# Kernel tuning notes

Measured on AMD Instinct MI355X. Metric: run time of the kernel, lower is better.

Reference implementation:

```python
import jax, jax.numpy as jnp
import numpy as np

B, S, D, H = 2, 2048, 1024, 16
HD = D // H
SCALE = HD ** -0.5


def setup_inputs() -> dict:
    key = jax.random.key(0)
    k1, k2, k3 = jax.random.split(key, 3)
    x = jax.random.normal(k1, (B, S, D), dtype=jnp.float32)
    # causal mask: True = masked (as used by masked_fill)
    mask = jnp.triu(jnp.ones((S, S), dtype=bool), k=1)
    w_qkv = jax.random.normal(k2, (D, 3 * D), dtype=jnp.float32) * (D ** -0.5)
    b_qkv = jnp.zeros((3 * D,), dtype=jnp.float32)
    w_out = jax.random.normal(k3, (D, D), dtype=jnp.float32) * (D ** -0.5)
    b_out = jnp.zeros((D,), dtype=jnp.float32)
    return {"x": x, "mask": mask, "w_qkv": w_qkv, "b_qkv": b_qkv,
            "w_out": w_out, "b_out": b_out}


def reference(x, mask, w_qkv, b_qkv, w_out, b_out):
    # qkv projection and split
    qkv = x @ w_qkv + b_qkv                     # [b, s, 3D]
    q, k, v = jnp.split(qkv, 3, axis=-1)
    # b s (h d) -> b h s d
    def to_heads(t):
        return t.reshape(B, S, H, HD).transpose(0, 2, 1, 3)
    q, k, v = to_heads(q), to_heads(k), to_heads(v)
    # attention scores [b, h, s, s]
    scores = jnp.einsum('bhqd,bhkd->bhqk', q, k) * SCALE
    scores = jnp.where(mask, -jnp.inf, scores)
    attn = jax.nn.softmax(scores, axis=-1)      # dropout is identity (eval)
    out = jnp.einsum('bhqk,bhkd->bhqd', attn, v)
    out = out.transpose(0, 2, 1, 3).reshape(B, S, D)  # b h s d -> b s (h d)
    out = out @ w_out + b_out                   # out dropout identity (eval)
    return (out, k, v)
```

## Files before the change

### kernel.cpp

```cpp
#include <hip/hip_runtime.h>
#include <hip/hip_bf16.h>

typedef short bf16x8 __attribute__((ext_vector_type(8)));
typedef short u16x4v __attribute__((ext_vector_type(4)));
typedef float f32x4  __attribute__((ext_vector_type(4)));
typedef unsigned short u16;
typedef unsigned int   u32;

#define NB   2
#define NS   2048
#define ND   1024
#define NH   16
#define NHD  64
#define N3   3072
#define NM   4096

__device__ __forceinline__ u16 f2bf(float f) {
    u32 u;
    __builtin_memcpy(&u, &f, 4);
    u += 0x7fffu + ((u >> 16) & 1u);
    return (u16)(u >> 16);
}
__device__ __forceinline__ bf16x8 load8f(const float* f) {
    float4 a = *(const float4*)f;
    float4 b = *(const float4*)(f + 4);
    bf16x8 r;
    r[0] = (short)f2bf(a.x); r[1] = (short)f2bf(a.y);
    r[2] = (short)f2bf(a.z); r[3] = (short)f2bf(a.w);
    r[4] = (short)f2bf(b.x); r[5] = (short)f2bf(b.y);
    r[6] = (short)f2bf(b.z); r[7] = (short)f2bf(b.w);
    return r;
}
__device__ __forceinline__ void gload_lds16(const void* g, void* l) {
    __builtin_amdgcn_global_load_lds(
        (const __attribute__((address_space(1))) u32*)g,
        (__attribute__((address_space(3))) u32*)l, 16, 0, 0);
}

__global__ __launch_bounds__(256) void prep_cvt(
    const float* __restrict__ X, u16* __restrict__ Xb,
    const float* __restrict__ Wqkv, u16* __restrict__ WqkvT,
    const float* __restrict__ Wout, u16* __restrict__ WoutT)
{
    __shared__ float t[32][33];
    const int b = blockIdx.x;
    if (b < 2048) {
        const int i = (b * 256 + threadIdx.x) * 8;
        *(bf16x8*)(Xb + i) = load8f(X + i);
        return;
    }
    const float* in; u16* outp; int R, C, tIdx;
    if (b < 5120) { in = Wqkv; outp = WqkvT; R = ND; C = N3; tIdx = b - 2048; }
    else          { in = Wout; outp = WoutT; R = ND; C = ND; tIdx = b - 5120; }
    const int nbc = C >> 5;
    const int r0 = (tIdx / nbc) << 5;
    const int c0 = (tIdx % nbc) << 5;
    const int tr = threadIdx.x >> 3, tc = (threadIdx.x & 7) << 2;
    const float4 v = *(const float4*)(in + (size_t)(r0 + tr) * C + c0 + tc);
    t[tr][tc] = v.x; t[tr][tc + 1] = v.y; t[tr][tc + 2] = v.z; t[tr][tc + 3] = v.w;
    __syncthreads();
    u16x4v ov;
    ov[0] = (short)f2bf(t[tc + 0][tr]); ov[1] = (short)f2bf(t[tc + 1][tr]);
    ov[2] = (short)f2bf(t[tc + 2][tr]); ov[3] = (short)f2bf(t[tc + 3][tr]);
    *(u16x4v*)(outp + (size_t)(c0 + tr) * R + r0 + tc) = ov;
}

template<bool BF>
__global__ __launch_bounds__(256) void qkv_gemm(
    const float* __restrict__ Xf, const u16* __restrict__ Xb,
    const float* __restrict__ Wf, const u16* __restrict__ WbT,
    const float* __restrict__ bias,
    u16* __restrict__ q_ws, u16* __restrict__ vT_ws, u16* __restrict__ k_ws,
    float* __restrict__ k_out, float* __restrict__ v_out)
{
    __shared__ __align__(16) u16 SM[128 * 128];
    u16* As = SM;
    u16* Bs = SM + 8192;

    const int bm = blockIdx.x & 31;
    const int bn = blockIdx.x >> 5;
    const int m0 = bm * 128, n0 = bn * 128;
    const int tid = threadIdx.x;
    const int lane = tid & 63, wv = tid >> 6;
    const int wm = wv >> 1, wn = wv & 1;
    const int li = lane & 15, lg = lane >> 4;
    const int gsw = ((lane & 7) * 16) ^ ((lane >> 3) << 4);
    const int rsw = (li & 7) << 3;

    f32x4 acc[4][4];
    #pragma unroll
    for (int i = 0; i < 4; ++i)
        #pragma unroll
        for (int j = 0; j < 4; ++j)
            acc[i][j] = (f32x4){0.f, 0.f, 0.f, 0.f};

    for (int k0 = 0; k0 < ND; k0 += 64) {
        if constexpr (BF) {
            #pragma unroll
            for (int i = 0; i < 4; ++i) {
                const int r0 = (i * 4 + wv) * 8;
                gload_lds16((const char*)(Xb  + (size_t)(m0 + r0 + (lane >> 3)) * ND + k0) + gsw, &As[r0 * 64]);
                gload_lds16((const char*)(WbT + (size_t)(n0 + r0 + (lane >> 3)) * ND + k0) + gsw, &Bs[r0 * 64]);
            }
        } else {
            #pragma unroll
            for (int i = 0; i < 4; ++i) {
                const int row = 32 * i + (tid >> 3), col = (tid & 7) * 8;
                *(bf16x8*)(&As[row * 64 + (col ^ ((row & 7) * 8))]) =
                    load8f(Xf + (size_t)(m0 + row) * ND + k0 + col);
            }
            #pragma unroll
            for (int i = 0; i < 4; ++i) {
                const int krow = 16 * i + (tid >> 4), ncol = (tid & 15) * 8;
                bf16x8 bv = load8f(Wf + (size_t)(k0 + krow) * N3 + n0 + ncol);
                #pragma unroll
                for (int jj = 0; jj < 8; ++jj) {
                    const int n_ = ncol + jj;
                    Bs[n_ * 64 + ((((krow >> 3) ^ (n_ & 7)) << 3) | (krow & 7))] = (u16)bv[jj];
                }
            }
        }
        __syncthreads();

        bf16x8 a[4][2], b[4][2];
        #pragma unroll
        for (int i = 0; i < 4; ++i)
            #pragma unroll
            for (int kk = 0; kk < 2; ++kk)
                a[i][kk] = *(const bf16x8*)(&As[(wm * 64 + i * 16 + li) * 64 + ((kk * 32 + lg * 8) ^ rsw)]);
        #pragma unroll
        for (int j = 0; j < 4; ++j)
            #pragma unroll
            for (int kk = 0; kk < 2; ++kk)
                b[j][kk] = *(const bf16x8*)(&Bs[(wn * 64 + j * 16 + li) * 64 + ((kk * 32 + lg * 8) ^ rsw)]);
        #pragma unroll
        for (int i = 0; i < 4; ++i)
            #pragma unroll
            for (int j = 0; j < 4; ++j) {
                acc[i][j] = __builtin_amdgcn_mfma_f32_16x16x32_bf16(a[i][0], b[j][0], acc[i][j], 0, 0, 0);
                acc[i][j] = __builtin_amdgcn_mfma_f32_16x16x32_bf16(a[i][1], b[j][1], acc[i][j], 0, 0, 0);
            }
        __syncthreads();
    }

    const int cls = bn >> 3;
    if (cls == 2) {
        #pragma unroll
        for (int i = 0; i < 4; ++i) {
          #pragma unroll
          for (int j = 0; j < 4; ++j) {
            const int gn = n0 + wn * 64 + j * 16 + li;
            const float bval = bias[gn];
            const int c = gn & 1023, h = c >> 6, d = c & 63;
            const int n_ = wn * 64 + j * 16 + li;
            #pragma unroll
            for (int r = 0; r < 4; ++r) {
                const int gm = m0 + wm * 64 + i * 16 + lg * 4 + r;
                const int b_ = gm >> 11, sI = gm & 2047;
                const float v = acc[i][j][r] + bval;
                v_out[(((size_t)(b_ * NH + h)) * NS + sI) * NHD + d] = v;
                const int m_ = wm * 64 + i * 16 + lg * 4 + r;
                SM[n_ * 128 + (m_ ^ ((n_ & 7) << 3))] = f2bf(v);
            }
          }
        }
        __syncthreads();
        const int nrow = tid >> 1, mh = tid & 1;
        const int cdx = (n0 - 2048) + nrow;
        const int hh = cdx >> 6, d = cdx & 63;
        const int b_ = m0 >> 11;
        const int s0 = (m0 & 2047) + mh * 64;
        u16* dst = vT_ws + (((size_t)(b_ * NH + hh)) * NHD + d) * NS + s0;
        #pragma unroll
        for (int c8 = 0; c8 < 8; ++c8) {
            const int m_ = mh * 64 + c8 * 8;
            *(bf16x8*)(dst + c8 * 8) =
                *(const bf16x8*)(&SM[nrow * 128 + (m_ ^ ((nrow & 7) << 3))]);
        }
    } else {
        #pragma unroll
        for (int i = 0; i < 4; ++i) {
          #pragma unroll
          for (int j = 0; j < 4; ++j) {
            const int gn = n0 + wn * 64 + j * 16 + li;
            const float bval = bias[gn];
            const int c = gn & 1023, h = c >> 6, d = c & 63;
            #pragma unroll
            for (int r = 0; r < 4; ++r) {
                const int gm = m0 + wm * 64 + i * 16 + lg * 4 + r;
                const int b_ = gm >> 11, sI = gm & 2047;
                const float v = acc[i][j][r] + bval;
                const size_t hidx = (((size_t)(b_ * NH + h)) * NS + sI) * NHD + d;
                if (cls == 0) {
                    q_ws[hidx] = f2bf(v * 0.125f);
                } else {
                    k_out[hidx] = v;
                    k_ws[hidx] = f2bf(v);
                }
            }
          }
        }
    }
}

__global__ __launch_bounds__(256, 4) void attn_fwd(
    u16* __restrict__ q_all, const u16* __restrict__ k_all,
    const u16* __restrict__ vT)
{
    __shared__ __align__(16) u16 Ks[2][64 * 64];
    __shared__ __align__(16) u16 Vs[2][64 * 64];
    __shared__ __align__(16) u16 Pl[4][16 * 64];

    const int tid = threadIdx.x;
    const int wv = tid >> 6, lane = tid & 63;
    const int li = lane & 15, lg = lane >> 4;
    const int bid = blockIdx.x;
    const int xcd = bid & 7, j = bid >> 3;
    const int bh  = (xcd << 2) | (j >> 5);
    const int jj  = j & 31;
    const int qt  = (j & 32) ? (31 - jj) : jj;
    const int q0  = qt * 64 + wv * 16;
    const int ntiles = qt + 1;

    u16* qp = q_all + (size_t)bh * NS * NHD;
    const u16* kp = k_all + (size_t)bh * NS * NHD;
    const u16* vp = vT + (size_t)bh * NHD * NS;

    const int rl = lane >> 3;
    const int gsw = ((lane & 7) * 16) ^ (rl << 4);
    const int rs = (li & 7) << 3;

    bf16x8 aq0 = *(const bf16x8*)(qp + (size_t)(q0 + li) * NHD + lg * 8);
    bf16x8 aq1 = *(const bf16x8*)(qp + (size_t)(q0 + li) * NHD + 32 + lg * 8);

    f32x4 o[4], ls;
    ls = (f32x4){0.f, 0.f, 0.f, 0.f};
    #pragma unroll
    for (int nf = 0; nf < 4; ++nf) o[nf] = (f32x4){0.f, 0.f, 0.f, 0.f};
    float m = 4.0f;

    const short onb = (short)0x3F80;
    const bf16x8 ones = {onb, onb, onb, onb, onb, onb, onb, onb};

    #define STAGE(B, KB) do {                                                           \
        _Pragma("unroll")                                                               \
        for (int i_ = 0; i_ < 2; ++i_) {                                                \
            const int row_ = 16 * wv + 8 * i_;                                          \
            gload_lds16((const char*)(kp + (size_t)((KB) + row_ + rl) * NHD) + gsw,     \
                        &Ks[B][row_ * 64]);                                             \
            gload_lds16((const char*)(vp + (size_t)(row_ + rl) * NS + (KB)) + gsw,      \
                        &Vs[B][row_ * 64]);                                             \
        } } while (0)

    STAGE(0, 0);
    __syncthreads();

    int buf = 0;
    for (int kt = 0; kt < ntiles; ++kt) {
        const int kb = kt * 64;
        if (kt + 1 < ntiles) STAGE(buf ^ 1, kb + 64);

        const u16* K = Ks[buf];
        const u16* V = Vs[buf];

        f32x4 s[4];
        __builtin_amdgcn_s_setprio(1);
        #pragma unroll
        for (int kq = 0; kq < 4; ++kq) {
            const u16* Kr = K + (kq * 16 + li) * 64;
            const bf16x8 b0 = *(const bf16x8*)(Kr + ((lg * 8) ^ rs));
            const bf16x8 b1 = *(const bf16x8*)(Kr + ((lg * 8 + 32) ^ rs));
            f32x4 t = (f32x4){0.f, 0.f, 0.f, 0.f};
            t = __builtin_amdgcn_mfma_f32_16x16x32_bf16(aq0, b0, t, 0, 0, 0);
            s[kq] = __builtin_amdgcn_mfma_f32_16x16x32_bf16(aq1, b1, t, 0, 0, 0);
        }
        __builtin_amdgcn_s_setprio(0);

        float mx = s[0][0];
        #pragma unroll
        for (int kq = 0; kq < 4; ++kq)
            #pragma unroll
            for (int r = 0; r < 4; ++r)
                mx = fmaxf(mx, s[kq][r]);
        if (__any(mx > m)) {
            #pragma unroll
            for (int dd = 1; dd < 64; dd <<= 1)
                mx = fmaxf(mx, __shfl_xor(mx, dd, 64));
            const float corr = __expf(m - mx);
            m = mx;
            #pragma unroll
            for (int nf = 0; nf < 4; ++nf)
                #pragma unroll
                for (int r = 0; r < 4; ++r) o[nf][r] *= corr;
            #pragma unroll
            for (int r = 0; r < 4; ++r) ls[r] *= corr;
        }

        bf16x8 vf[4][2];
        #pragma unroll
        for (int nf = 0; nf < 4; ++nf) {
            const u16* Vr = V + (nf * 16 + li) * 64;
            vf[nf][0] = *(const bf16x8*)(Vr + ((lg * 8) ^ rs));
            vf[nf][1] = *(const bf16x8*)(Vr + ((lg * 8 + 32) ^ rs));
        }

        const bool maskt = (kt == ntiles - 1);
        u16* PW = Pl[wv];
        #pragma unroll
        for (int r = 0; r < 4; ++r) {
            const int q_ = lg * 4 + r;
            const int qrow = q0 + q_;
            const int qm = q_ & 7;
            #pragma unroll
            for (int kq = 0; kq < 4; ++kq) {
                float ev = __expf(s[kq][r] - m);
                if (maskt && (kb + kq * 16 + li > qrow)) ev = 0.f;
                PW[q_ * 64 + ((((2 * kq + (li >> 3)) ^ qm) << 3) | (li & 7))] = f2bf(ev);
            }
        }
        asm volatile("s_waitcnt lgkmcnt(0)" ::: "memory");
        const bf16x8 pa0 = *(const bf16x8*)(PW + li * 64 + ((lg ^ (li & 7)) << 3));
        const bf16x8 pa1 = *(const bf16x8*)(PW + li * 64 + (((lg + 4) ^ (li & 7)) << 3));
        __builtin_amdgcn_s_setprio(1);
        #pragma unroll
        for (int nf = 0; nf < 4; ++nf) {
            f32x4 t = __builtin_amdgcn_mfma_f32_16x16x32_bf16(pa0, vf[nf][0], o[nf], 0, 0, 0);
            o[nf] = __builtin_amdgcn_mfma_f32_16x16x32_bf16(pa1, vf[nf][1], t, 0, 0, 0);
        }
        ls = __builtin_amdgcn_mfma_f32_16x16x32_bf16(pa0, ones, ls, 0, 0, 0);
        ls = __builtin_amdgcn_mfma_f32_16x16x32_bf16(pa1, ones, ls, 0, 0, 0);
        __builtin_amdgcn_s_setprio(0);

        __syncthreads();
        buf ^= 1;
    }

    #pragma unroll
    for (int nf = 0; nf < 4; ++nf)
        #pragma unroll
        for (int r = 0; r < 4; ++r)
            qp[(size_t)(q0 + lg * 4 + r) * NHD + nf * 16 + li] = f2bf(o[nf][r] / ls[r]);
    #undef STAGE
}

template<bool BF>
__global__ __launch_bounds__(256) void out_gemm(
    const u16* __restrict__ Aq,
    const float* __restrict__ Wf, const u16* __restrict__ WbT,
    const float* __restrict__ bias, float* __restrict__ outp)
{
    __shared__ __align__(16) u16 As[128 * 64];
    __shared__ __align__(16) u16 Bs[128 * 64];

    const int bm = blockIdx.x & 31;
    const int bn = blockIdx.x >> 5;
    const int m0 = bm * 128, n0 = bn * 128;
    const int tid = threadIdx.x;
    const int lane = tid & 63, wv = tid >> 6;
    const int wm = wv >> 1, wn = wv & 1;
    const int li = lane & 15, lg = lane >> 4;
    const int gsw = ((lane & 7) * 16) ^ ((lane >> 3) << 4);
    const int rsw = (li & 7) << 3;

    f32x4 acc[4][4];
    #pragma unroll
    for (int i = 0; i < 4; ++i)
        #pragma unroll
        for (int j = 0; j < 4; ++j)
            acc[i][j] = (f32x4){0.f, 0.f, 0.f, 0.f};

    for (int k0 = 0; k0 < ND; k0 += 64) {
        const int h = k0 >> 6;
        #pragma unroll
        for (int i = 0; i < 4; ++i) {
            const int r0 = (i * 4 + wv) * 8;
            const int gm = m0 + r0 + (lane >> 3);
            const int b_ = gm >> 11, sI = gm & 2047;
            gload_lds16((const char*)(Aq + (((size_t)(b_ * NH + h)) * NS + sI) * NHD) + gsw,
                        &As[r0 * 64]);
            if constexpr (BF)
                gload_lds16((const char*)(WbT + (size_t)(n0 + r0 + (lane >> 3)) * ND + k0) + gsw,
                            &Bs[r0 * 64]);
        }
        if constexpr (!BF) {
            #pragma unroll
            for (int i = 0; i < 4; ++i) {
                const int krow = 16 * i + (tid >> 4), ncol = (tid & 15) * 8;
                bf16x8 bv = load8f(Wf + (size_t)(k0 + krow) * ND + n0 + ncol);
                #pragma unroll
                for (int jj = 0; jj < 8; ++jj) {
                    const int n_ = ncol + jj;
                    Bs[n_ * 64 + ((((krow >> 3) ^ (n_ & 7)) << 3) | (krow & 7))] = (u16)bv[jj];
                }
            }
        }
        __syncthreads();

        bf16x8 a[4][2], b[4][2];
        #pragma unroll
        for (int i = 0; i < 4; ++i)
            #pragma unroll
            for (int kk = 0; kk < 2; ++kk)
                a[i][kk] = *(const bf16x8*)(&As[(wm * 64 + i * 16 + li) * 64 + ((kk * 32 + lg * 8) ^ rsw)]);
        #pragma unroll
        for (int j = 0; j < 4; ++j)
            #pragma unroll
            for (int kk = 0; kk < 2; ++kk)
                b[j][kk] = *(const bf16x8*)(&Bs[(wn * 64 + j * 16 + li) * 64 + ((kk * 32 + lg * 8) ^ rsw)]);
        #pragma unroll
        for (int i = 0; i < 4; ++i)
            #pragma unroll
            for (int j = 0; j < 4; ++j) {
                acc[i][j] = __builtin_amdgcn_mfma_f32_16x16x32_bf16(a[i][0], b[j][0], acc[i][j], 0, 0, 0);
                acc[i][j] = __builtin_amdgcn_mfma_f32_16x16x32_bf16(a[i][1], b[j][1], acc[i][j], 0, 0, 0);
            }
        __syncthreads();
    }

    #pragma unroll
    for (int i = 0; i < 4; ++i) {
      #pragma unroll
      for (int j = 0; j < 4; ++j) {
        const int gn = n0 + wn * 64 + j * 16 + li;
        const float bval = bias[gn];
        #pragma unroll
        for (int r = 0; r < 4; ++r) {
            const int gm = m0 + wm * 64 + i * 16 + lg * 4 + r;
            outp[(size_t)gm * ND + gn] = acc[i][j][r] + bval;
        }
      }
    }
}

extern "C" void kernel_launch(void* const* d_in, const int* in_sizes, int n_in,
                              void* d_out, int out_size, void* d_ws, size_t ws_size,
                              hipStream_t stream)
{
    const float* X    = (const float*)d_in[0];
    const float* Wqkv = (const float*)d_in[2];
    const float* bqkv = (const float*)d_in[3];
    const float* Wout = (const float*)d_in[4];
    const float* bout = (const float*)d_in[5];

    const size_t HE = (size_t)NB * NH * NS * NHD;

    float* out  = (float*)d_out;
    float* kout = out + HE;
    float* vout = kout + HE;

    u16* q_ws  = (u16*)d_ws;
    u16* vT_ws = q_ws + HE;
    u16* k_ws  = vT_ws + HE;

    u16* Xb     = k_ws + HE;
    u16* WqkvT  = Xb + (size_t)NM * ND;
    u16* WoutT  = WqkvT + (size_t)ND * N3;
    const bool big = ws_size >= (size_t)41943040;

    if (big) {
        prep_cvt<<<dim3(6144), dim3(256), 0, stream>>>(X, Xb, Wqkv, WqkvT, Wout, WoutT);
        qkv_gemm<true><<<dim3(32 * 24), dim3(256), 0, stream>>>(
            X, Xb, Wqkv, WqkvT, bqkv, q_ws, vT_ws, k_ws, kout, vout);
    } else {
        qkv_gemm<false><<<dim3(32 * 24), dim3(256), 0, stream>>>(
            X, Xb, Wqkv, WqkvT, bqkv, q_ws, vT_ws, k_ws, kout, vout);
    }

    attn_fwd<<<dim3(1024), dim3(256), 0, stream>>>(q_ws, k_ws, vT_ws);

    if (big) {
        out_gemm<true><<<dim3(32 * 8), dim3(256), 0, stream>>>(
            q_ws, Wout, WoutT, bout, out);
    } else {
        out_gemm<false><<<dim3(32 * 8), dim3(256), 0, stream>>>(
            q_ws, Wout, WoutT, bout, out);
    }
}
```

Before: 126.0 us.

## Double-buffer LDS tiles in QKV and output GEMMs to overlap loads with MFMA

Measured after the change: 115.1 us (median of 2 runs). 8.6% less time.

```diff
diff --git a/kernel.cpp b/kernel.cpp
--- a/kernel.cpp
+++ b/kernel.cpp
@@ -73,9 +73,8 @@
     u16* __restrict__ q_ws, u16* __restrict__ vT_ws, u16* __restrict__ k_ws,
     float* __restrict__ k_out, float* __restrict__ v_out)
 {
-    __shared__ __align__(16) u16 SM[128 * 128];
-    u16* As = SM;
-    u16* Bs = SM + 8192;
+    __shared__ __align__(16) u16 As[2][128 * 64];
+    __shared__ __align__(16) u16 Bs[2][128 * 64];
 
     const int bm = blockIdx.x & 31;
     const int bn = blockIdx.x >> 5;
@@ -94,19 +93,19 @@
         for (int j = 0; j < 4; ++j)
             acc[i][j] = (f32x4){0.f, 0.f, 0.f, 0.f};
 
-    for (int k0 = 0; k0 < ND; k0 += 64) {
+    auto stage = [&](int B, int k0) {
         if constexpr (BF) {
             #pragma unroll
             for (int i = 0; i < 4; ++i) {
                 const int r0 = (i * 4 + wv) * 8;
-                gload_lds16((const char*)(Xb  + (size_t)(m0 + r0 + (lane >> 3)) * ND + k0) + gsw, &As[r0 * 64]);
-                gload_lds16((const char*)(WbT + (size_t)(n0 + r0 + (lane >> 3)) * ND + k0) + gsw, &Bs[r0 * 64]);
+                gload_lds16((const char*)(Xb  + (size_t)(m0 + r0 + (lane >> 3)) * ND + k0) + gsw, &As[B][r0 * 64]);
+                gload_lds16((const char*)(WbT + (size_t)(n0 + r0 + (lane >> 3)) * ND + k0) + gsw, &Bs[B][r0 * 64]);
             }
         } else {
             #pragma unroll
             for (int i = 0; i < 4; ++i) {
                 const int row = 32 * i + (tid >> 3), col = (tid & 7) * 8;
-                *(bf16x8*)(&As[row * 64 + (col ^ ((row & 7) * 8))]) =
+                *(bf16x8*)(&As[B][row * 64 + (col ^ ((row & 7) * 8))]) =
                     load8f(Xf + (size_t)(m0 + row) * ND + k0 + col);
             }
             #pragma unroll
@@ -116,23 +115,31 @@
                 #pragma unroll
                 for (int jj = 0; jj < 8; ++jj) {
                     const int n_ = ncol + jj;
-                    Bs[n_ * 64 + ((((krow >> 3) ^ (n_ & 7)) << 3) | (krow & 7))] = (u16)bv[jj];
+                    Bs[B][n_ * 64 + ((((krow >> 3) ^ (n_ & 7)) << 3) | (krow & 7))] = (u16)bv[jj];
                 }
             }
         }
-        __syncthreads();
+    };
+
+    stage(0, 0);
+    __syncthreads();
+
+    int buf = 0;
+    for (int k0 = 0; k0 < ND; k0 += 64) {
+        if (k0 + 64 < ND) stage(buf ^ 1, k0 + 64);
 
         bf16x8 a[4][2], b[4][2];
         #pragma unroll
         for (int i = 0; i < 4; ++i)
             #pragma unroll
             for (int kk = 0; kk < 2; ++kk)
-                a[i][kk] = *(const bf16x8*)(&As[(wm * 64 + i * 16 + li) * 64 + ((kk * 32 + lg * 8) ^ rsw)]);
+                a[i][kk] = *(const bf16x8*)(&As[buf][(wm * 64 + i * 16 + li) * 64 + ((kk * 32 + lg * 8) ^ rsw)]);
         #pragma unroll
         for (int j = 0; j < 4; ++j)
             #pragma unroll
             for (int kk = 0; kk < 2; ++kk)
-                b[j][kk] = *(const bf16x8*)(&Bs[(wn * 64 + j * 16 + li) * 64 + ((kk * 32 + lg * 8) ^ rsw)]);
+                b[j][kk] = *(const bf16x8*)(&Bs[buf][(wn * 64 + j * 16 + li) * 64 + ((kk * 32 + lg * 8) ^ rsw)]);
+        __builtin_amdgcn_s_setprio(1);
         #pragma unroll
         for (int i = 0; i < 4; ++i)
             #pragma unroll
@@ -140,11 +147,15 @@
                 acc[i][j] = __builtin_amdgcn_mfma_f32_16x16x32_bf16(a[i][0], b[j][0], acc[i][j], 0, 0, 0);
                 acc[i][j] = __builtin_amdgcn_mfma_f32_16x16x32_bf16(a[i][1], b[j][1], acc[i][j], 0, 0, 0);
             }
+        __builtin_amdgcn_s_setprio(0);
+
         __syncthreads();
+        buf ^= 1;
     }
 
     const int cls = bn >> 3;
     if (cls == 2) {
+        u16* SM = &As[0][0];
         #pragma unroll
         for (int i = 0; i < 4; ++i) {
           #pragma unroll
@@ -349,8 +360,8 @@
     const float* __restrict__ Wf, const u16* __restrict__ WbT,
     const float* __restrict__ bias, float* __restrict__ outp)
 {
-    __shared__ __align__(16) u16 As[128 * 64];
-    __shared__ __align__(16) u16 Bs[128 * 64];
+    __shared__ __align__(16) u16 As[2][128 * 64];
+    __shared__ __align__(16) u16 Bs[2][128 * 64];
 
     const int bm = blockIdx.x & 31;
     const int bn = blockIdx.x >> 5;
@@ -369,7 +380,7 @@
         for (int j = 0; j < 4; ++j)
             acc[i][j] = (f32x4){0.f, 0.f, 0.f, 0.f};
 
-    for (int k0 = 0; k0 < ND; k0 += 64) {
+    auto stage = [&](int B, int k0) {
         const int h = k0 >> 6;
         #pragma unroll
         for (int i = 0; i < 4; ++i) {
@@ -377,10 +388,10 @@
             const int gm = m0 + r0 + (lane >> 3);
             const int b_ = gm >> 11, sI = gm & 2047;
             gload_lds16((const char*)(Aq + (((size_t)(b_ * NH + h)) * NS + sI) * NHD) + gsw,
-                        &As[r0 * 64]);
+                        &As[B][r0 * 64]);
             if constexpr (BF)
                 gload_lds16((const char*)(WbT + (size_t)(n0 + r0 + (lane >> 3)) * ND + k0) + gsw,
-                            &Bs[r0 * 64]);
+                            &Bs[B][r0 * 64]);
         }
         if constexpr (!BF) {
             #pragma unroll
@@ -390,23 +401,31 @@
                 #pragma unroll
                 for (int jj = 0; jj < 8; ++jj) {
                     const int n_ = ncol + jj;
-                    Bs[n_ * 64 + ((((krow >> 3) ^ (n_ & 7)) << 3) | (krow & 7))] = (u16)bv[jj];
+                    Bs[B][n_ * 64 + ((((krow >> 3) ^ (n_ & 7)) << 3) | (krow & 7))] = (u16)bv[jj];
                 }
             }
         }
-        __syncthreads();
+    };
+
+    stage(0, 0);
+    __syncthreads();
+
+    int buf = 0;
+    for (int k0 = 0; k0 < ND; k0 += 64) {
+        if (k0 + 64 < ND) stage(buf ^ 1, k0 + 64);
 
         bf16x8 a[4][2], b[4][2];
         #pragma unroll
         for (int i = 0; i < 4; ++i)
             #pragma unroll
             for (int kk = 0; kk < 2; ++kk)
-                a[i][kk] = *(const bf16x8*)(&As[(wm * 64 + i * 16 + li) * 64 + ((kk * 32 + lg * 8) ^ rsw)]);
+                a[i][kk] = *(const bf16x8*)(&As[buf][(wm * 64 + i * 16 + li) * 64 + ((kk * 32 + lg * 8) ^ rsw)]);
         #pragma unroll
         for (int j = 0; j < 4; ++j)
             #pragma unroll
             for (int kk = 0; kk < 2; ++kk)
-                b[j][kk] = *(const bf16x8*)(&Bs[(wn * 64 + j * 16 + li) * 64 + ((kk * 32 + lg * 8) ^ rsw)]);
+                b[j][kk] = *(const bf16x8*)(&Bs[buf][(wn * 64 + j * 16 + li) * 64 + ((kk * 32 + lg * 8) ^ rsw)]);
+        __builtin_amdgcn_s_setprio(1);
         #pragma unroll
         for (int i = 0; i < 4; ++i)
             #pragma unroll
@@ -414,7 +433,10 @@
                 acc[i][j] = __builtin_amdgcn_mfma_f32_16x16x32_bf16(a[i][0], b[j][0], acc[i][j], 0, 0, 0);
                 acc[i][j] = __builtin_amdgcn_mfma_f32_16x16x32_bf16(a[i][1], b[j][1], acc[i][j], 0, 0, 0);
             }
+        __builtin_amdgcn_s_setprio(0);
+
         __syncthreads();
+        buf ^= 1;
     }
 
     #pragma unroll
```
